# Optimization experiments

Measured on AMD Instinct MI355X. Metric: run time of the kernel, lower is better.

## Reference

```python
import jax, jax.numpy as jnp
import numpy as np

B, T, H = 8, 2048, 512


def _minimaxn(x):
    # global min-max normalization (NetTransform.minimaxn)
    mx = jnp.max(x)
    mn = jnp.min(x)
    return (x - mn) / (mx - mn)


def _fb(e):
    # NetTransform.fb, mode='batch', vectorized over the batch.
    # e: (B, 1, T) -> (B, 1, T, T)
    # Result: out[b,0,i,j] = prod(e[b,0,j:i]) for i>j, 1 on diag, 0 above diag.
    x = e[:, 0]                                   # (B, T)
    Bsz, Tsz = x.shape
    X = jnp.broadcast_to(x[:, :, None], (Bsz, Tsz, Tsz))  # xs = x.unsqueeze(-1).repeat(1,1,T)
    tril1 = jnp.tril(jnp.ones((Tsz, Tsz), x.dtype))
    m_f = jnp.triu(jnp.ones((Tsz, Tsz), x.dtype), 1)
    A = X * tril1 + m_f                           # tril(x) + m_f
    C = jnp.cumprod(A, axis=1)                    # cumprod along dim -2
    S = jnp.concatenate([jnp.ones((Bsz, 1, Tsz), x.dtype), C[:, :-1]], axis=1) - m_f
    return S[:, None]                             # (B, 1, T, T)


def _clustering(energy_t):
    # NetTransform.clustering (tnum == 1), vectorized over batch.
    # energy_t: (B, 1, T) -> bool mask (B, 1, T) with top-num_neg of (1-energy) set True
    x = 1.0 - energy_t[:, 0]                      # (B, T)
    num_neg = x.sum(-1).astype(jnp.int32)         # int() truncation; x >= 0 so == floor
    ranks = jnp.argsort(jnp.argsort(-x, axis=-1), axis=-1)  # rank 0 = largest
    m = ranks < num_neg[:, None]
    return m[:, None]                             # (B, 1, T)


def setup_inputs() -> dict:
    key = jax.random.key(0)
    k1, k2, k3 = jax.random.split(key, 3)
    e = jax.random.uniform(k1, (B, 1, T), dtype=jnp.float32)
    h = jax.random.normal(k2, (B, 1, T, H), dtype=jnp.float32)
    ilens = jnp.concatenate([
        jnp.array([T], dtype=jnp.int32),
        jax.random.randint(k3, (B - 1,), T // 2, T + 1).astype(jnp.int32),
    ])
    return {"e": e, "h": h, "ilens": ilens}


def reference(e, h, ilens):
    sg = jax.lax.stop_gradient
    # energy_t = minimaxn(flows['e']).detach()
    energy_t = sg(_minimaxn(e))                   # (B, 1, T)
    # clustering mask (computed in forward; unused when cutting_gauge == 0)
    _ = _clustering(energy_t)
    # energy_t_cumprod = fb(energy_t)  (under no_grad)
    K = sg(_fb(energy_t))                         # (B, 1, T, T)
    # h_agg = (K @ h) / K.sum(-1, keepdim), then transpose(-2, -1)
    h_agg = jnp.einsum('bnts,bnsh->bnth', K, h) / K.sum(-1, keepdims=True)
    h_agg = jnp.swapaxes(h_agg, -2, -1)           # (B, 1, H, T)
    # kernel = (h @ h_agg.detach() + h.detach() @ h_agg) / 2 / sqrt(H)
    kernel = (jnp.matmul(h, sg(h_agg)) + jnp.matmul(sg(h), h_agg)) / 2.0 / np.sqrt(H).astype(np.float32)
    return kernel                                 # (B, 1, T, T)
```

## Files before the change

kernel.cpp:

```cpp
#include <hip/hip_runtime.h>
#include <hip/hip_bf16.h>
#include <stdint.h>

#define B_DIM 8
#define T_DIM 2048
#define H_DIM 512
#define NC 32
#define LCH 64
#define NSUB 4
#define LSUB 16
#define NSEG (NC * NSUB)
#define BM 128
#define BN 128
#define BK 64

typedef float floatx4 __attribute__((ext_vector_type(4)));
typedef __bf16 bf16x4 __attribute__((ext_vector_type(4)));
typedef __bf16 bf16x8 __attribute__((ext_vector_type(8)));

__global__ __launch_bounds__(1024) void minmax_kernel(const float* __restrict__ e,
                                                      float* __restrict__ stats) {
    const float4* e4 = (const float4*)e;
    int tid = threadIdx.x;
    float mn = 1e30f, mx = -1e30f;
    #pragma unroll
    for (int i = 0; i < 4; ++i) {
        float4 v = e4[tid + i * 1024];
        mn = fminf(mn, fminf(fminf(v.x, v.y), fminf(v.z, v.w)));
        mx = fmaxf(mx, fmaxf(fmaxf(v.x, v.y), fmaxf(v.z, v.w)));
    }
    for (int off = 32; off > 0; off >>= 1) {
        mn = fminf(mn, __shfl_down(mn, off, 64));
        mx = fmaxf(mx, __shfl_down(mx, off, 64));
    }
    __shared__ float smn[16], smx[16];
    int wid = tid >> 6;
    if ((tid & 63) == 0) { smn[wid] = mn; smx[wid] = mx; }
    __syncthreads();
    if (tid == 0) {
        mn = smn[0]; mx = smx[0];
        #pragma unroll
        for (int w = 1; w < 16; ++w) { mn = fminf(mn, smn[w]); mx = fmaxf(mx, smx[w]); }
        stats[0] = mn;
        stats[1] = 1.0f / (mx - mn);
    }
}

__global__ __launch_bounds__(512) void chunk_sum_kernel(
        const float* __restrict__ e, const float* __restrict__ h,
        const float* __restrict__ stats,
        __hip_bfloat16* __restrict__ h_bf,
        float* __restrict__ Lsub, float* __restrict__ PPsub, float* __restrict__ LDsub) {
    const int b = blockIdx.x, c = blockIdx.y;
    const int tid = threadIdx.x;
    const int hdq = tid & 127, sub = tid >> 7;
    const int hd = hdq * 4;
    const int t0 = c * LCH + sub * LSUB;

    __shared__ float se[LCH];
    if (tid < LCH) {
        int t = c * LCH + tid;
        se[tid] = (t == 0) ? 0.0f : (e[b * T_DIM + t - 1] - stats[0]) * stats[1];
    }
    __syncthreads();

    const float* hp = h + ((size_t)b * T_DIM + t0) * H_DIM + hd;
    __hip_bfloat16* hbp = h_bf + ((size_t)b * T_DIM + t0) * H_DIM + hd;

    floatx4 lv = {0.0f, 0.0f, 0.0f, 0.0f};
    float ldv = 0.0f, pp = 1.0f;
    #pragma unroll 8
    for (int i = 0; i < LSUB; ++i) {
        float a = se[sub * LSUB + i];
        floatx4 hv = *(const floatx4*)(hp + (size_t)i * H_DIM);
        lv = a * lv + hv;
        ldv = fmaf(a, ldv, 1.0f);
        pp *= a;
        bf16x4 o;
        #pragma unroll
        for (int k = 0; k < 4; ++k) o[k] = (__bf16)hv[k];
        *(bf16x4*)(hbp + (size_t)i * H_DIM) = o;
    }
    int seg = (b * NC + c) * NSUB + sub;
    *(floatx4*)(Lsub + (size_t)seg * H_DIM + hd) = lv;
    if (hdq == 0) { PPsub[seg] = pp; LDsub[seg] = ldv; }
}

__global__ __launch_bounds__(512) void carry_kernel(
        const float* __restrict__ Lsub, const float* __restrict__ PPsub,
        const float* __restrict__ LDsub,
        float* __restrict__ Ssub, float* __restrict__ SDsub) {
    const int b = blockIdx.x, hd = threadIdx.x;
    float s = 0.0f, sd = 0.0f;
    #pragma unroll 4
    for (int g = 0; g < NSEG; ++g) {
        int seg = b * NSEG + g;
        Ssub[(size_t)seg * H_DIM + hd] = s;
        if (hd == 0) SDsub[seg] = sd;
        float pe = PPsub[seg];
        s  = fmaf(pe, s,  Lsub[(size_t)seg * H_DIM + hd]);
        sd = fmaf(pe, sd, LDsub[seg]);
    }
}

__global__ __launch_bounds__(512) void rescan_kernel(
        const float* __restrict__ e, const __hip_bfloat16* __restrict__ h_bf,
        const float* __restrict__ stats,
        const float* __restrict__ Ssub, const float* __restrict__ SDsub,
        __hip_bfloat16* __restrict__ hagg_bf) {
    const int b = blockIdx.x, c = blockIdx.y;
    const int tid = threadIdx.x;
    const int hdq = tid & 127, sub = tid >> 7;
    const int hd = hdq * 4;
    const int t0 = c * LCH + sub * LSUB;

    __shared__ float se[LCH];
    if (tid < LCH) {
        int t = c * LCH + tid;
        se[tid] = (t == 0) ? 0.0f : (e[b * T_DIM + t - 1] - stats[0]) * stats[1];
    }
    __syncthreads();

    const int seg = (b * NC + c) * NSUB + sub;
    const __hip_bfloat16* hbp = h_bf + ((size_t)b * T_DIM + t0) * H_DIM + hd;
    __hip_bfloat16* hop = hagg_bf + ((size_t)b * T_DIM + t0) * H_DIM + hd;

    floatx4 s = *(const floatx4*)(Ssub + (size_t)seg * H_DIM + hd);
    float sd = SDsub[seg];
    #pragma unroll 8
    for (int i = 0; i < LSUB; ++i) {
        float a = se[sub * LSUB + i];
        bf16x4 hb = *(const bf16x4*)(hbp + (size_t)i * H_DIM);
        floatx4 hv;
        #pragma unroll
        for (int k = 0; k < 4; ++k) hv[k] = (float)hb[k];
        s = a * s + hv;
        sd = fmaf(a, sd, 1.0f);
        float inv = 1.0f / sd;
        bf16x4 o;
        #pragma unroll
        for (int k = 0; k < 4; ++k) o[k] = (__bf16)(s[k] * inv);
        *(bf16x4*)(hop + (size_t)i * H_DIM) = o;
    }
}

__device__ __forceinline__ void async16(const void* g, void* l) {
    __builtin_amdgcn_global_load_lds(
        (__attribute__((address_space(1))) void*)g,
        (__attribute__((address_space(3))) void*)l,
        16, 0, 0);
}

__global__ __launch_bounds__(256) void gemm_kernel(
        const __hip_bfloat16* __restrict__ Abf,
        const __hip_bfloat16* __restrict__ Bbf,
        float* __restrict__ C) {
    __shared__ __align__(16) __hip_bfloat16 As[BM * BK];
    __shared__ __align__(16) __hip_bfloat16 Bs[BN * BK];

    const int id = blockIdx.x + (blockIdx.y << 4) + (blockIdx.z << 8);
    const int b  = id & 7;
    const int tt = id >> 3;
    const int tm = (tt & 15) * BM;
    const int sn = (tt >> 4) * BN;

    const int tid = threadIdx.x;
    const int lane = tid & 63;
    const int wave = tid >> 6;
    const int wm = (wave >> 1) * 64;
    const int wn = (wave & 1) * 64;
    const int l16 = lane & 15;
    const int quad = lane >> 4;

    const int srow = tid >> 3;
    const int sgran = (tid & 7) ^ (srow & 7);
    const __hip_bfloat16* Ag = Abf + ((size_t)b * T_DIM + tm + srow) * H_DIM + sgran * 8;
    const __hip_bfloat16* Bg = Bbf + ((size_t)b * T_DIM + sn + srow) * H_DIM + sgran * 8;
    char* AsB = (char*)As;
    char* BsB = (char*)Bs;

    floatx4 zero = {0.0f, 0.0f, 0.0f, 0.0f};
    floatx4 acc[4][4];
    #pragma unroll
    for (int i = 0; i < 4; ++i)
        #pragma unroll
        for (int j = 0; j < 4; ++j) acc[i][j] = zero;

    for (int kk = 0; kk < H_DIM; kk += BK) {
        __syncthreads();
        #pragma unroll
        for (int q = 0; q < 4; ++q) {
            async16(Ag + (size_t)q * 32 * H_DIM + kk, AsB + q * 4096 + tid * 16);
            async16(Bg + (size_t)q * 32 * H_DIM + kk, BsB + q * 4096 + tid * 16);
        }
        asm volatile("s_waitcnt vmcnt(0)" ::: "memory");
        __syncthreads();

        bf16x8 af[2][4], bfv[2][4];
        #pragma unroll
        for (int ku = 0; ku < 2; ++ku)
            #pragma unroll
            for (int i = 0; i < 4; ++i) {
                int ra = wm + i * 16 + l16;
                int rb = wn + i * 16 + l16;
                int ga = (ku * 4 + quad) ^ (l16 & 7);
                af[ku][i]  = *reinterpret_cast<const bf16x8*>(AsB + ra * 128 + ga * 16);
                bfv[ku][i] = *reinterpret_cast<const bf16x8*>(BsB + rb * 128 + ga * 16);
            }
        #pragma unroll
        for (int ku = 0; ku < 2; ++ku)
            #pragma unroll
            for (int i = 0; i < 4; ++i)
                #pragma unroll
                for (int j = 0; j < 4; ++j)
                    acc[i][j] = __builtin_amdgcn_mfma_f32_16x16x32_bf16(bfv[ku][j], af[ku][i], acc[i][j], 0, 0, 0);
    }

    const float scale = 0.04419417382415922f;
    float* Cp = C + (size_t)b * T_DIM * T_DIM;
    #pragma unroll
    for (int i = 0; i < 4; ++i) {
        int row = tm + wm + i * 16 + l16;
        float* crow = Cp + (size_t)row * T_DIM;
        #pragma unroll
        for (int j = 0; j < 4; ++j) {
            int col = sn + wn + j * 16 + quad * 4;
            floatx4 v;
            #pragma unroll
            for (int r = 0; r < 4; ++r) v[r] = acc[i][j][r] * scale;
            *(floatx4*)(crow + col) = v;
        }
    }
}

extern "C" void kernel_launch(void* const* d_in, const int* in_sizes, int n_in,
                              void* d_out, int out_size, void* d_ws, size_t ws_size,
                              hipStream_t stream) {
    const float* e = (const float*)d_in[0];
    const float* h = (const float*)d_in[1];
    float* out = (float*)d_out;

    char* ws = (char*)d_ws;
    float* stats            = (float*)ws;
    __hip_bfloat16* h_bf    = (__hip_bfloat16*)(ws + 4096);
    __hip_bfloat16* hagg_bf = (__hip_bfloat16*)(ws + 4096 + (16u << 20));
    char* p = ws + 4096 + (32u << 20);
    float* Lsub  = (float*)p;   p += (size_t)B_DIM * NSEG * H_DIM * 4;
    float* Ssub  = (float*)p;   p += (size_t)B_DIM * NSEG * H_DIM * 4;
    float* PPsub = (float*)p;   p += B_DIM * NSEG * 4;
    float* LDsub = (float*)p;   p += B_DIM * NSEG * 4;
    float* SDsub = (float*)p;

    minmax_kernel<<<1, 1024, 0, stream>>>(e, stats);
    chunk_sum_kernel<<<dim3(B_DIM, NC), 512, 0, stream>>>(e, h, stats, h_bf, Lsub, PPsub, LDsub);
    carry_kernel<<<B_DIM, 512, 0, stream>>>(Lsub, PPsub, LDsub, Ssub, SDsub);
    rescan_kernel<<<dim3(B_DIM, NC), 512, 0, stream>>>(e, h_bf, stats, Ssub, SDsub, hagg_bf);
    gemm_kernel<<<dim3(T_DIM / BM, T_DIM / BN, B_DIM), 256, 0, stream>>>(h_bf, hagg_bf, out);
}
```

Baseline: 237.0 us.

## Enlarge GEMM tiles to 256x256 with double-buffered async LDS loads

The GEMM block tile grows from 128x128 to 256x256 with 512 threads (8 waves, each computing 128x64). The K loop becomes double-buffered in 128KB of LDS, so the next K slab is prefetched while MFMAs run on the current one, and s_setprio raises wave priority around the MFMA bursts. This targets global-load latency and per-tile data reuse. In exchange, the block count drops to 512 (one block per CU because of LDS use), and each thread holds twice as many accumulators, which raises register pressure.

```diff
diff --git a/kernel.cpp b/kernel.cpp
--- a/kernel.cpp
+++ b/kernel.cpp
@@ -10,8 +10,8 @@
 #define NSUB 4
 #define LSUB 16
 #define NSEG (NC * NSUB)
-#define BM 128
-#define BN 128
+#define BM 256
+#define BN 256
 #define BK 64
 
 typedef float floatx4 __attribute__((ext_vector_type(4)));
@@ -151,24 +151,25 @@
         16, 0, 0);
 }
 
-__global__ __launch_bounds__(256) void gemm_kernel(
+__global__ __launch_bounds__(512) void gemm_kernel(
         const __hip_bfloat16* __restrict__ Abf,
         const __hip_bfloat16* __restrict__ Bbf,
         float* __restrict__ C) {
-    __shared__ __align__(16) __hip_bfloat16 As[BM * BK];
-    __shared__ __align__(16) __hip_bfloat16 Bs[BN * BK];
-
-    const int id = blockIdx.x + (blockIdx.y << 4) + (blockIdx.z << 8);
+    __shared__ __align__(16) char lds[131072];
+    char* AsB = lds;
+    char* BsB = lds + 65536;
+
+    const int id = blockIdx.x + (blockIdx.y << 3) + (blockIdx.z << 6);
     const int b  = id & 7;
     const int tt = id >> 3;
-    const int tm = (tt & 15) * BM;
-    const int sn = (tt >> 4) * BN;
+    const int tm = (tt & 7) * BM;
+    const int sn = (tt >> 3) * BN;
 
     const int tid = threadIdx.x;
     const int lane = tid & 63;
     const int wave = tid >> 6;
-    const int wm = (wave >> 1) * 64;
-    const int wn = (wave & 1) * 64;
+    const int wm = (wave >> 2) * 128;
+    const int wn = (wave & 3) * 64;
     const int l16 = lane & 15;
     const int quad = lane >> 4;
 
@@ -176,50 +177,76 @@
     const int sgran = (tid & 7) ^ (srow & 7);
     const __hip_bfloat16* Ag = Abf + ((size_t)b * T_DIM + tm + srow) * H_DIM + sgran * 8;
     const __hip_bfloat16* Bg = Bbf + ((size_t)b * T_DIM + sn + srow) * H_DIM + sgran * 8;
-    char* AsB = (char*)As;
-    char* BsB = (char*)Bs;
 
     floatx4 zero = {0.0f, 0.0f, 0.0f, 0.0f};
-    floatx4 acc[4][4];
+    floatx4 acc[8][4];
     #pragma unroll
-    for (int i = 0; i < 4; ++i)
+    for (int i = 0; i < 8; ++i)
         #pragma unroll
         for (int j = 0; j < 4; ++j) acc[i][j] = zero;
 
-    for (int kk = 0; kk < H_DIM; kk += BK) {
-        __syncthreads();
-        #pragma unroll
-        for (int q = 0; q < 4; ++q) {
-            async16(Ag + (size_t)q * 32 * H_DIM + kk, AsB + q * 4096 + tid * 16);
-            async16(Bg + (size_t)q * 32 * H_DIM + kk, BsB + q * 4096 + tid * 16);
+    #define STAGE(kt, buf) do {                                                        \
+        const int kk_ = (kt) * BK;                                                     \
+        _Pragma("unroll")                                                              \
+        for (int q = 0; q < 4; ++q) {                                                  \
+            async16(Ag + (size_t)(q * 64) * H_DIM + kk_,                               \
+                    AsB + (buf) * 32768 + q * 8192 + tid * 16);                        \
+            async16(Bg + (size_t)(q * 64) * H_DIM + kk_,                               \
+                    BsB + (buf) * 32768 + q * 8192 + tid * 16);                        \
+        }                                                                              \
+    } while (0)
+
+    STAGE(0, 0);
+
+    for (int t = 0; t < H_DIM / BK; ++t) {
+        const int cur = t & 1;
+        if (t < H_DIM / BK - 1) {
+            STAGE(t + 1, cur ^ 1);
+            asm volatile("s_waitcnt vmcnt(8)" ::: "memory");
+        } else {
+            asm volatile("s_waitcnt vmcnt(0)" ::: "memory");
         }
-        asm volatile("s_waitcnt vmcnt(0)" ::: "memory");
-        __syncthreads();
-
-        bf16x8 af[2][4], bfv[2][4];
-        #pragma unroll
-        for (int ku = 0; ku < 2; ++ku)
+        __builtin_amdgcn_s_barrier();
+
+        const char* Ab = AsB + cur * 32768;
+        const char* Bb = BsB + cur * 32768;
+        #pragma unroll
+        for (int ku = 0; ku < 2; ++ku) {
+            bf16x8 bv[4];
             #pragma unroll
-            for (int i = 0; i < 4; ++i) {
-                int ra = wm + i * 16 + l16;
-                int rb = wn + i * 16 + l16;
-                int ga = (ku * 4 + quad) ^ (l16 & 7);
-                af[ku][i]  = *reinterpret_cast<const bf16x8*>(AsB + ra * 128 + ga * 16);
-                bfv[ku][i] = *reinterpret_cast<const bf16x8*>(BsB + rb * 128 + ga * 16);
+            for (int j = 0; j < 4; ++j) {
+                int rb = wn + j * 16 + l16;
+                int gb = (ku * 4 + quad) ^ (l16 & 7);
+                bv[j] = *reinterpret_cast<const bf16x8*>(Bb + rb * 128 + gb * 16);
             }
-        #pragma unroll
-        for (int ku = 0; ku < 2; ++ku)
             #pragma unroll
-            for (int i = 0; i < 4; ++i)
+            for (int ih = 0; ih < 2; ++ih) {
+                bf16x8 av[4];
                 #pragma unroll
-                for (int j = 0; j < 4; ++j)
-                    acc[i][j] = __builtin_amdgcn_mfma_f32_16x16x32_bf16(bfv[ku][j], af[ku][i], acc[i][j], 0, 0, 0);
-    }
+                for (int i2 = 0; i2 < 4; ++i2) {
+                    int ra = wm + (ih * 4 + i2) * 16 + l16;
+                    int ga = (ku * 4 + quad) ^ (l16 & 7);
+                    av[i2] = *reinterpret_cast<const bf16x8*>(Ab + ra * 128 + ga * 16);
+                }
+                __builtin_amdgcn_s_setprio(1);
+                #pragma unroll
+                for (int i2 = 0; i2 < 4; ++i2)
+                    #pragma unroll
+                    for (int j = 0; j < 4; ++j)
+                        acc[ih * 4 + i2][j] = __builtin_amdgcn_mfma_f32_16x16x32_bf16(
+                            bv[j], av[i2], acc[ih * 4 + i2][j], 0, 0, 0);
+                __builtin_amdgcn_s_setprio(0);
+            }
+        }
+        asm volatile("s_waitcnt lgkmcnt(0)" ::: "memory");
+        __builtin_amdgcn_s_barrier();
+    }
+    #undef STAGE
 
     const float scale = 0.04419417382415922f;
     float* Cp = C + (size_t)b * T_DIM * T_DIM;
     #pragma unroll
-    for (int i = 0; i < 4; ++i) {
+    for (int i = 0; i < 8; ++i) {
         int row = tm + wm + i * 16 + l16;
         float* crow = Cp + (size_t)row * T_DIM;
         #pragma unroll
@@ -255,5 +282,5 @@
     chunk_sum_kernel<<<dim3(B_DIM, NC), 512, 0, stream>>>(e, h, stats, h_bf, Lsub, PPsub, LDsub);
     carry_kernel<<<B_DIM, 512, 0, stream>>>(Lsub, PPsub, LDsub, Ssub, SDsub);
     rescan_kernel<<<dim3(B_DIM, NC), 512, 0, stream>>>(e, h_bf, stats, Ssub, SDsub, hagg_bf);
-    gemm_kernel<<<dim3(T_DIM / BM, T_DIM / BN, B_DIM), 256, 0, stream>>>(h_bf, hagg_bf, out);
-}
+    gemm_kernel<<<dim3(8, 8, B_DIM), 512, 0, stream>>>(h_bf, hagg_bf, out);
+}
```

New measurement: 242.3 us. 2.2% more time.

## Split serial carry scan into three-level hierarchical scan across more blocks

Applied to the files above, without the earlier changes.

Replaces the single carry kernel, which runs 8 blocks each walking 128 segments serially, with three kernels. The first reduces groups of 16 segments in parallel over 64 blocks, the second scans the 8 group totals per batch, and the third expands the carries back out to each segment in parallel. The aim is to shorten the serial dependency chain and use more CUs. In exchange it adds two kernel launches and some extra memory traffic.

```diff
diff --git a/kernel.cpp b/kernel.cpp
--- a/kernel.cpp
+++ b/kernel.cpp
@@ -10,6 +10,7 @@
 #define NSUB 4
 #define LSUB 16
 #define NSEG (NC * NSUB)
+#define NOCT 8
 #define BM 128
 #define BN 128
 #define BK 64
@@ -86,15 +87,54 @@
     if (hdq == 0) { PPsub[seg] = pp; LDsub[seg] = ldv; }
 }
 
-__global__ __launch_bounds__(512) void carry_kernel(
+__global__ __launch_bounds__(512) void octet_kernel(
         const float* __restrict__ Lsub, const float* __restrict__ PPsub,
         const float* __restrict__ LDsub,
-        float* __restrict__ Ssub, float* __restrict__ SDsub) {
+        float* __restrict__ Loct, float* __restrict__ Poct, float* __restrict__ LDoct) {
+    const int b = blockIdx.x, o = blockIdx.y, hd = threadIdx.x;
+    float lc = 0.0f, ldc = 0.0f, P = 1.0f;
+    #pragma unroll 4
+    for (int i = 0; i < 16; ++i) {
+        int seg = b * NSEG + o * 16 + i;
+        float pe = PPsub[seg];
+        lc  = fmaf(pe, lc,  Lsub[(size_t)seg * H_DIM + hd]);
+        ldc = fmaf(pe, ldc, LDsub[seg]);
+        P *= pe;
+    }
+    int oc = b * NOCT + o;
+    Loct[(size_t)oc * H_DIM + hd] = lc;
+    if (hd == 0) { Poct[oc] = P; LDoct[oc] = ldc; }
+}
+
+__global__ __launch_bounds__(512) void octfold_kernel(
+        const float* __restrict__ Loct, const float* __restrict__ Poct,
+        const float* __restrict__ LDoct,
+        float* __restrict__ Soct, float* __restrict__ SDoct) {
     const int b = blockIdx.x, hd = threadIdx.x;
     float s = 0.0f, sd = 0.0f;
+    #pragma unroll
+    for (int o = 0; o < NOCT; ++o) {
+        int oc = b * NOCT + o;
+        Soct[(size_t)oc * H_DIM + hd] = s;
+        if (hd == 0) SDoct[oc] = sd;
+        float P = Poct[oc];
+        s  = fmaf(P, s,  Loct[(size_t)oc * H_DIM + hd]);
+        sd = fmaf(P, sd, LDoct[oc]);
+    }
+}
+
+__global__ __launch_bounds__(512) void segfold_kernel(
+        const float* __restrict__ Lsub, const float* __restrict__ PPsub,
+        const float* __restrict__ LDsub,
+        const float* __restrict__ Soct, const float* __restrict__ SDoct,
+        float* __restrict__ Ssub, float* __restrict__ SDsub) {
+    const int b = blockIdx.x, o = blockIdx.y, hd = threadIdx.x;
+    int oc = b * NOCT + o;
+    float s = Soct[(size_t)oc * H_DIM + hd];
+    float sd = SDoct[oc];
     #pragma unroll 4
-    for (int g = 0; g < NSEG; ++g) {
-        int seg = b * NSEG + g;
+    for (int i = 0; i < 16; ++i) {
+        int seg = b * NSEG + o * 16 + i;
         Ssub[(size_t)seg * H_DIM + hd] = s;
         if (hd == 0) SDsub[seg] = sd;
         float pe = PPsub[seg];
@@ -249,11 +289,18 @@
     float* Ssub  = (float*)p;   p += (size_t)B_DIM * NSEG * H_DIM * 4;
     float* PPsub = (float*)p;   p += B_DIM * NSEG * 4;
     float* LDsub = (float*)p;   p += B_DIM * NSEG * 4;
-    float* SDsub = (float*)p;
+    float* SDsub = (float*)p;   p += B_DIM * NSEG * 4;
+    float* Loct  = (float*)p;   p += (size_t)B_DIM * NOCT * H_DIM * 4;
+    float* Soct  = (float*)p;   p += (size_t)B_DIM * NOCT * H_DIM * 4;
+    float* Poct  = (float*)p;   p += B_DIM * NOCT * 4;
+    float* LDoct = (float*)p;   p += B_DIM * NOCT * 4;
+    float* SDoct = (float*)p;
 
     minmax_kernel<<<1, 1024, 0, stream>>>(e, stats);
     chunk_sum_kernel<<<dim3(B_DIM, NC), 512, 0, stream>>>(e, h, stats, h_bf, Lsub, PPsub, LDsub);
-    carry_kernel<<<B_DIM, 512, 0, stream>>>(Lsub, PPsub, LDsub, Ssub, SDsub);
+    octet_kernel<<<dim3(B_DIM, NOCT), 512, 0, stream>>>(Lsub, PPsub, LDsub, Loct, Poct, LDoct);
+    octfold_kernel<<<B_DIM, 512, 0, stream>>>(Loct, Poct, LDoct, Soct, SDoct);
+    segfold_kernel<<<dim3(B_DIM, NOCT), 512, 0, stream>>>(Lsub, PPsub, LDsub, Soct, SDoct, Ssub, SDsub);
     rescan_kernel<<<dim3(B_DIM, NC), 512, 0, stream>>>(e, h_bf, stats, Ssub, SDsub, hagg_bf);
     gemm_kernel<<<dim3(T_DIM / BM, T_DIM / BN, B_DIM), 256, 0, stream>>>(h_bf, hagg_bf, out);
 }
```

New measurement: 209.4 us. -11.6%, faster.
